# Kernel tuning notes

Hardware: AMD Instinct MI355X
Metric: run time of the kernel (lower is better)

## Reference

```python
import jax, jax.numpy as jnp
import numpy as np

EMBED = 256
HEADS = 8
LEVELS = 4
POINTS = 8
CAMS = 6
D_HEAD = EMBED // HEADS  # 32
SHAPES = [(92, 160), (46, 80), (23, 40), (12, 20)]  # (H, W) per level, L = 19560


def setup_inputs() -> dict:
    key = jax.random.key(0)
    ks = jax.random.split(key, 12)
    bs, nq, Z = 1, 2500, 4
    L = sum(h * w for h, w in SHAPES)

    def lin(k, fan_in, fan_out, scale=1.0):
        return jax.random.normal(k, (fan_in, fan_out), jnp.float32) * (scale / np.sqrt(fan_in).astype(np.float32))

    return dict(
        query=jax.random.normal(ks[0], (bs, nq, EMBED), jnp.float32),
        key_feats=jax.random.normal(ks[1], (CAMS, L, bs, EMBED), jnp.float32),
        reference_points_cam=jax.random.uniform(ks[2], (CAMS, bs, nq, Z, 2), jnp.float32),
        bev_mask=jax.random.bernoulli(ks[3], 0.3, (CAMS, bs, nq, Z)),
        spatial_shapes=jnp.array(SHAPES, dtype=jnp.int32),
        W_value=lin(ks[4], EMBED, EMBED),
        b_value=jnp.zeros((EMBED,), jnp.float32),
        W_off=lin(ks[5], EMBED, HEADS * LEVELS * POINTS * 2, 0.1),
        b_off=jnp.zeros((HEADS * LEVELS * POINTS * 2,), jnp.float32),
        W_attn=lin(ks[6], EMBED, HEADS * LEVELS * POINTS),
        b_attn=jnp.zeros((HEADS * LEVELS * POINTS,), jnp.float32),
        W_out=lin(ks[7], EMBED, EMBED),
        b_out=jnp.zeros((EMBED,), jnp.float32),
    )


def _deform_attn(q, val, ref, W_off, b_off, W_attn, b_attn):
    """MSDeformableAttention3D core. q: (Bc,Nq,C), val: (Bc,L,H,d) [already value-projected],
    ref: (Bc,Nq,Z,2) normalized camera-plane points."""
    Bc, Nq, C = q.shape
    Z = ref.shape[2]
    # sampling offsets, normalized per level by (W, H)
    off = (q @ W_off + b_off).reshape(Bc, Nq, HEADS, LEVELS, POINTS, 2)
    norm = jnp.array([[w, h] for h, w in SHAPES], jnp.float32)  # (Lv, 2) as (W, H)
    off = off / norm[None, None, None, :, None, :]
    # BEVFormer 3D combination: broadcast offsets over the Z pillar anchors
    off = off.reshape(Bc, Nq, HEADS, LEVELS, POINTS // Z, Z, 2)
    loc = ref[:, :, None, None, None, :, :] + off  # (Bc,Nq,H,Lv,P/Z,Z,2)
    loc = loc.reshape(Bc, Nq, HEADS, LEVELS, POINTS, 2)
    # attention weights softmaxed jointly over (levels*points)
    aw = jax.nn.softmax((q @ W_attn + b_attn).reshape(Bc, Nq, HEADS, LEVELS * POINTS), axis=-1)
    aw = aw.reshape(Bc, Nq, HEADS, LEVELS, POINTS)

    val_t = val.transpose(0, 2, 1, 3)  # (Bc,H,L,d)
    gather = jax.vmap(jax.vmap(lambda vm, im: vm[im]))  # over Bc and H
    out = jnp.zeros((Bc, HEADS, Nq, D_HEAD), jnp.float32)
    start = 0
    for lvl, (Hh, Ww) in enumerate(SHAPES):
        v_l = val_t[:, :, start:start + Hh * Ww]  # (Bc,H,HW,d)
        start += Hh * Ww
        # grid_sample semantics, align_corners=False, zero padding
        x = loc[:, :, :, lvl, :, 0] * Ww - 0.5  # (Bc,Nq,H,P)
        y = loc[:, :, :, lvl, :, 1] * Hh - 0.5
        x0 = jnp.floor(x)
        y0 = jnp.floor(y)
        fx = x - x0
        fy = y - y0
        a_l = aw[:, :, :, lvl]  # (Bc,Nq,H,P)
        for dy in (0, 1):
            for dx in (0, 1):
                xi = x0 + dx
                yi = y0 + dy
                wgt = (fx if dx else 1.0 - fx) * (fy if dy else 1.0 - fy)
                valid = (xi >= 0) & (xi < Ww) & (yi >= 0) & (yi < Hh)
                idx = (jnp.clip(yi, 0, Hh - 1) * Ww + jnp.clip(xi, 0, Ww - 1)).astype(jnp.int32)
                cw = jnp.where(valid, wgt * a_l, 0.0).transpose(0, 2, 1, 3)  # (Bc,H,Nq,P)
                g = gather(v_l, idx.transpose(0, 2, 1, 3))  # (Bc,H,Nq,P,d)
                out = out + jnp.einsum('bhnp,bhnpd->bhnd', cw, g)
    return out.transpose(0, 2, 1, 3).reshape(Bc, Nq, C)


def reference(query, key_feats, reference_points_cam, bev_mask, spatial_shapes,
              W_value, b_value, W_off, b_off, W_attn, b_attn, W_out, b_out):
    bs, nq, C = query.shape
    # Rebatch equivalent: every camera sees all queries; invalid ones are masked out
    # after the (fully per-query) deformable attention, which matches the original
    # gather->pad->attend->scatter math exactly.
    q_bc = jnp.broadcast_to(query[:, None], (bs, CAMS, nq, C)).reshape(bs * CAMS, nq, C)
    v = key_feats.transpose(2, 0, 1, 3).reshape(bs * CAMS, -1, C)  # (Bc,L,C)
    val = (v @ W_value + b_value).reshape(bs * CAMS, -1, HEADS, D_HEAD)
    ref = reference_points_cam.transpose(1, 0, 2, 3, 4).reshape(bs * CAMS, nq, -1, 2)
    out = _deform_attn(q_bc, val, ref, W_off, b_off, W_attn, b_attn)  # (Bc,nq,C)
    out = out.reshape(bs, CAMS, nq, C)
    valid_q = bev_mask.sum(-1) > 0  # (CAMS, bs, nq)
    mask = valid_q.transpose(1, 0, 2).astype(query.dtype)  # (bs, CAMS, nq)
    slots = jnp.einsum('bcq,bcqd->bqd', mask, out)
    count = jnp.maximum(mask.sum(1), 1.0)  # (bs, nq)
    slots = slots / count[..., None]
    return slots @ W_out + b_out + query
```

## Files before the change

### kernel.cpp

```cpp
#include <hip/hip_runtime.h>
#include <hip/hip_bf16.h>
#include <cstdint>

#define NCAMS 6
#define NQ 2500
#define EMBED 256
#define HEADS 8
#define DHEAD 32
#define LTOT 19560
#define MVAL (NCAMS * LTOT)

typedef __attribute__((ext_vector_type(8))) short bf16x8;
typedef __attribute__((ext_vector_type(4))) float f32x4;

__device__ __forceinline__ unsigned short f2bf(float f) {
  unsigned u = __float_as_uint(f);
  return (unsigned short)((u + 0x7fffu + ((u >> 16) & 1u)) >> 16);
}
__device__ __forceinline__ unsigned short bfbits(float x) {
  __hip_bfloat16 h = __float2bfloat16(x);
  return __builtin_bit_cast(unsigned short, h);
}
__device__ __forceinline__ void gl16(const unsigned short* g, unsigned short* l) {
  __builtin_amdgcn_global_load_lds(
      (const __attribute__((address_space(1))) unsigned int*)g,
      (__attribute__((address_space(3))) unsigned int*)l, 16, 0, 0);
}

__global__ __launch_bounds__(256) void k_prep(
    const float* __restrict__ Wv, const float* __restrict__ Woff,
    const float* __restrict__ Wattn, const float* __restrict__ Wout,
    const float* __restrict__ query,
    unsigned short* __restrict__ WT, unsigned short* __restrict__ WTq,
    unsigned short* __restrict__ WoutT, unsigned short* __restrict__ qbf)
{
  const int b = blockIdx.x, t = threadIdx.x;
  if (b < 256) {
    WT[(size_t)b * 256 + t] = f2bf(Wv[(size_t)t * 256 + b]);
  } else if (b < 768) {
    int c = b - 256;
    WTq[(size_t)c * 256 + t] = f2bf(Woff[(size_t)t * 512 + c]);
  } else if (b < 1024) {
    int c = b - 768;
    WTq[(size_t)(512 + c) * 256 + t] = f2bf(Wattn[(size_t)t * 256 + c]);
  } else if (b < 1280) {
    int c = b - 1024;
    WoutT[(size_t)c * 256 + t] = f2bf(Wout[(size_t)t * 256 + c]);
  } else {
    int q = b - 1280;
    qbf[(size_t)q * 256 + t] = f2bf(query[(size_t)q * 256 + t]);
  }
}

__global__ __launch_bounds__(256) void k_abf(
    const float* __restrict__ A, unsigned short* __restrict__ Abf)
{
  const size_t N8 = (size_t)MVAL * 256 / 8;
  for (size_t i = (size_t)blockIdx.x * 256 + threadIdx.x; i < N8;
       i += (size_t)gridDim.x * 256) {
    float4 x = *(const float4*)&A[i * 8];
    float4 y = *(const float4*)&A[i * 8 + 4];
    uint4 u;
    u.x = (unsigned)f2bf(x.x) | ((unsigned)f2bf(x.y) << 16);
    u.y = (unsigned)f2bf(x.z) | ((unsigned)f2bf(x.w) << 16);
    u.z = (unsigned)f2bf(y.x) | ((unsigned)f2bf(y.y) << 16);
    u.w = (unsigned)f2bf(y.z) | ((unsigned)f2bf(y.w) << 16);
    *(uint4*)&Abf[i * 8] = u;
  }
}

__global__ __launch_bounds__(512, 2) void k_valproj(
    const unsigned short* __restrict__ Abf,
    const unsigned short* __restrict__ WT,
    const float* __restrict__ bv,
    unsigned short* __restrict__ val)
{
  __shared__ unsigned short smem[128 * 64 + 256 * 64];
  unsigned short* As = smem;
  unsigned short* Bs = smem + 128 * 64;
  const int t = threadIdx.x;
  const int lane = t & 63;
  const int wid = t >> 6;
  const int wm = wid >> 2, wn = wid & 3;
  const int laneM = lane & 15, kGrp = lane >> 4;
  const int bm = blockIdx.x * 128;

  const int sub = t >> 3;
  const int swz = (t & 7) ^ (sub & 7);
  const unsigned short* aS0 = Abf + (size_t)min(bm + sub, MVAL - 1) * 256 + swz * 8;
  const unsigned short* aS1 = Abf + (size_t)min(bm + 64 + sub, MVAL - 1) * 256 + swz * 8;
  const unsigned short* bS0 = WT + (size_t)(sub) * 256 + swz * 8;
  const unsigned short* bS1 = WT + (size_t)(64 + sub) * 256 + swz * 8;
  const unsigned short* bS2 = WT + (size_t)(128 + sub) * 256 + swz * 8;
  const unsigned short* bS3 = WT + (size_t)(192 + sub) * 256 + swz * 8;

  f32x4 acc[4][4];
#pragma unroll
  for (int m = 0; m < 4; ++m)
#pragma unroll
    for (int n = 0; n < 4; ++n) acc[m][n] = {0.f, 0.f, 0.f, 0.f};

#pragma unroll 1
  for (int kk = 0; kk < 4; ++kk) {
    if (kk) __syncthreads();
    const int ko = kk * 64;
    gl16(aS0 + ko, As + wid * 512);
    gl16(aS1 + ko, As + 4096 + wid * 512);
    gl16(bS0 + ko, Bs + wid * 512);
    gl16(bS1 + ko, Bs + 4096 + wid * 512);
    gl16(bS2 + ko, Bs + 8192 + wid * 512);
    gl16(bS3 + ko, Bs + 12288 + wid * 512);
    __syncthreads();

#pragma unroll
    for (int ks = 0; ks < 2; ++ks) {
      bf16x8 af[4], bfr[4];
#pragma unroll
      for (int m = 0; m < 4; ++m) {
        int row = wm * 64 + m * 16 + laneM;
        af[m] = *(bf16x8*)&As[row * 64 + (((ks * 4 + kGrp) ^ (row & 7)) << 3)];
      }
#pragma unroll
      for (int n = 0; n < 4; ++n) {
        int row = wn * 64 + n * 16 + laneM;
        bfr[n] = *(bf16x8*)&Bs[row * 64 + (((ks * 4 + kGrp) ^ (row & 7)) << 3)];
      }
#pragma unroll
      for (int m = 0; m < 4; ++m)
#pragma unroll
        for (int n = 0; n < 4; ++n)
          acc[m][n] = __builtin_amdgcn_mfma_f32_16x16x32_bf16(bfr[n], af[m], acc[m][n], 0, 0, 0);
    }
  }

  float4 bb4[4];
#pragma unroll
  for (int n = 0; n < 4; ++n)
    bb4[n] = *(const float4*)&bv[wn * 64 + n * 16 + kGrp * 4];

  __syncthreads();
  unsigned short* tlw = smem + wid * (32 * 72);

#pragma unroll
  for (int hm = 0; hm < 2; ++hm) {
#pragma unroll
    for (int mm = 0; mm < 2; ++mm) {
      const int m = hm * 2 + mm;
#pragma unroll
      for (int n = 0; n < 4; ++n) {
        uint2 u;
        u.x = (unsigned)bfbits(acc[m][n][0] + bb4[n].x) |
              ((unsigned)bfbits(acc[m][n][1] + bb4[n].y) << 16);
        u.y = (unsigned)bfbits(acc[m][n][2] + bb4[n].z) |
              ((unsigned)bfbits(acc[m][n][3] + bb4[n].w) << 16);
        *(uint2*)&tlw[(mm * 16 + laneM) * 72 + n * 16 + kGrp * 4] = u;
      }
    }
#pragma unroll
    for (int i = 0; i < 4; ++i) {
      const int rowl = i * 8 + (lane >> 3);
      const int c8 = lane & 7;
      uint4 v = *(const uint4*)&tlw[rowl * 72 + c8 * 8];
      const int row = bm + wm * 64 + hm * 32 + rowl;
      if (row < MVAL)
        *(uint4*)&val[(size_t)row * 256 + wn * 64 + c8 * 8] = v;
    }
  }
}

__global__ __launch_bounds__(256, 2) void k_gemm_small(
    const unsigned short* __restrict__ A,
    const unsigned short* __restrict__ BT,
    const float* __restrict__ ba, const float* __restrict__ bb, int bsplit,
    const float* __restrict__ resid,
    float* __restrict__ C, int M, int N, int withResid)
{
  __shared__ unsigned short As[128 * 64];
  __shared__ unsigned short Bs[128 * 64];
  const int t = threadIdx.x;
  const int lane = t & 63;
  const int wid = t >> 6;
  const int wm = wid >> 1, wn = wid & 1;
  const int laneM = lane & 15, kGrp = lane >> 4;
  const int bm = blockIdx.x * 128;
  const int bn = blockIdx.y * 128;

  const int aC = t & 7, aR0 = t >> 3;

  uint4 aRegs[2][4];
  uint4 bRegs[2][4];
  f32x4 acc[4][4];
#pragma unroll
  for (int m = 0; m < 4; ++m)
#pragma unroll
    for (int n = 0; n < 4; ++n) acc[m][n] = {0.f, 0.f, 0.f, 0.f};

#pragma unroll
  for (int p = 0; p < 4; ++p) {
    int arow = bm + aR0 + p * 32;
    aRegs[0][p] = (arow < M) ? *(const uint4*)&A[(size_t)arow * 256 + aC * 8]
                             : make_uint4(0u, 0u, 0u, 0u);
    bRegs[0][p] = *(const uint4*)&BT[(size_t)(bn + aR0 + p * 32) * 256 + aC * 8];
  }

#pragma unroll
  for (int kk = 0; kk < 4; ++kk) {
    const int cur = kk & 1, nxt = cur ^ 1;
    if (kk) __syncthreads();
#pragma unroll
    for (int p = 0; p < 4; ++p) {
      int row = aR0 + p * 32;
      int elem = row * 64 + ((aC ^ (row & 7)) << 3);
      *(uint4*)&As[elem] = aRegs[cur][p];
      *(uint4*)&Bs[elem] = bRegs[cur][p];
    }
    __syncthreads();
    if (kk < 3) {
      const int kn = (kk + 1) * 64;
#pragma unroll
      for (int p = 0; p < 4; ++p) {
        int arow = bm + aR0 + p * 32;
        aRegs[nxt][p] = (arow < M)
            ? *(const uint4*)&A[(size_t)arow * 256 + kn + aC * 8]
            : make_uint4(0u, 0u, 0u, 0u);
        bRegs[nxt][p] = *(const uint4*)&BT[(size_t)(bn + aR0 + p * 32) * 256 + kn + aC * 8];
      }
    }
#pragma unroll
    for (int ks = 0; ks < 2; ++ks) {
      bf16x8 af[4], bfr[4];
#pragma unroll
      for (int m = 0; m < 4; ++m) {
        int row = wm * 64 + m * 16 + laneM;
        af[m] = *(bf16x8*)&As[row * 64 + (((ks * 4 + kGrp) ^ (row & 7)) << 3)];
      }
#pragma unroll
      for (int n = 0; n < 4; ++n) {
        int row = wn * 64 + n * 16 + laneM;
        bfr[n] = *(bf16x8*)&Bs[row * 64 + (((ks * 4 + kGrp) ^ (row & 7)) << 3)];
      }
#pragma unroll
      for (int m = 0; m < 4; ++m)
#pragma unroll
        for (int n = 0; n < 4; ++n)
          acc[m][n] = __builtin_amdgcn_mfma_f32_16x16x32_bf16(af[m], bfr[n], acc[m][n], 0, 0, 0);
    }
  }

  float bvn[4];
#pragma unroll
  for (int n = 0; n < 4; ++n) {
    int col = bn + wn * 64 + n * 16 + laneM;
    bvn[n] = (col < bsplit) ? ba[col] : bb[col - bsplit];
  }
#pragma unroll
  for (int m = 0; m < 4; ++m) {
#pragma unroll
    for (int r = 0; r < 4; ++r) {
      int row = bm + wm * 64 + m * 16 + kGrp * 4 + r;
      if (row < M) {
#pragma unroll
        for (int n = 0; n < 4; ++n) {
          int col = bn + wn * 64 + n * 16 + laneM;
          float v = acc[m][n][r] + bvn[n];
          if (withResid) v += resid[(size_t)row * 256 + col];
          C[(size_t)row * N + col] = v;
        }
      }
    }
  }
}

__global__ __launch_bounds__(256) void k_maskvalid(
    const unsigned char* __restrict__ MSK,
    unsigned char* __restrict__ valid)
{
  __shared__ int s_u8;
  const int t = threadIdx.x;
  if (t == 0) s_u8 = 0;
  __syncthreads();
  if ((t & 3) && MSK[t]) atomicOr(&s_u8, 1);
  __syncthreads();
  const int isU8 = s_u8;

  const int i = blockIdx.x * 256 + t;
  if (i < NCAMS * NQ) {
    int any;
    if (isU8) {
      const unsigned char* p = MSK + (size_t)i * 4;
      any = p[0] | p[1] | p[2] | p[3];
    } else {
      const int* p = (const int*)MSK + (size_t)i * 4;
      any = p[0] | p[1] | p[2] | p[3];
    }
    valid[i] = any ? 1 : 0;
  }
}

__global__ __launch_bounds__(256) void k_sample(
    const unsigned short* __restrict__ val,
    const float* __restrict__ OFFLOG,
    const float* __restrict__ REF,
    const unsigned char* __restrict__ valid,
    unsigned short* __restrict__ slots)
{
  __shared__ int2  s_pack[4][NCAMS][256];
  __shared__ float s_off[512];
  __shared__ float s_ref[48];
  __shared__ int   s_valid[6];

  const int q = blockIdx.x;
  const int t = threadIdx.x;

  s_off[t]       = OFFLOG[(size_t)q * 768 + t];
  s_off[t + 256] = OFFLOG[(size_t)q * 768 + 256 + t];
  if (t < 48) s_ref[t] = REF[(size_t)(t >> 3) * (NQ * 8) + (size_t)q * 8 + (t & 7)];
  if (t < 6) s_valid[t] = valid[(size_t)t * NQ + q];

  float logit = OFFLOG[(size_t)q * 768 + 512 + t];
  float m = logit;
#pragma unroll
  for (int o = 16; o > 0; o >>= 1) m = fmaxf(m, __shfl_xor(m, o, 32));
  float e = __expf(logit - m);
  float s = e;
#pragma unroll
  for (int o = 16; o > 0; o >>= 1) s += __shfl_xor(s, o, 32);
  const float a = e / s;
  __syncthreads();

  {
    const int h1 = t >> 5, lp = t & 31, lvl = lp >> 3, p = lp & 7, z = p & 3;
    const int WW = 160 >> lvl;
    const int HH = (lvl < 3) ? (92 >> lvl) : 12;
    const int S  = (lvl == 0) ? 0 : (lvl == 1) ? 14720 : (lvl == 2) ? 18400 : 19320;
    const float Wf = (float)WW, Hf = (float)HH;
    const float ox = s_off[h1 * 64 + lp * 2];
    const float oy = s_off[h1 * 64 + lp * 2 + 1];
#pragma unroll 1
    for (int cam = 0; cam < NCAMS; ++cam) {
      if (!s_valid[cam]) continue;
      float rx = s_ref[cam * 8 + z * 2];
      float ry = s_ref[cam * 8 + z * 2 + 1];
      float x = rx * Wf + ox - 0.5f;
      float y = ry * Hf + oy - 0.5f;
      float x0f = floorf(x), y0f = floorf(y);
      float fx = x - x0f, fy = y - y0f;
      int x0 = (int)x0f, y0 = (int)y0f;
      int base = cam * LTOT + S;
#pragma unroll
      for (int dy = 0; dy < 2; ++dy) {
        int yi = y0 + dy;
        float wy = dy ? fy : 1.f - fy;
        int yc = min(max(yi, 0), HH - 1);
        bool vy = (yi >= 0) && (yi < HH);
#pragma unroll
        for (int dx = 0; dx < 2; ++dx) {
          int xi = x0 + dx;
          float wx = dx ? fx : 1.f - fx;
          int xc = min(max(xi, 0), WW - 1);
          bool vv = vy && (xi >= 0) && (xi < WW);
          float wgt = vv ? wx * wy * a : 0.f;
          int addr = (base + yc * WW + xc) * 512;
          s_pack[dy * 2 + dx][cam][t] = make_int2(addr, __float_as_int(wgt));
        }
      }
    }
  }
  __syncthreads();

  const int h = t >> 5, pp = (t >> 3) & 3, l8 = t & 7;
  const unsigned dconst = (unsigned)(h * 64 + l8 * 8);
  const char* vb = (const char*)val;
  int nvalid = s_valid[0] + s_valid[1] + s_valid[2] + s_valid[3] + s_valid[4] + s_valid[5];
  float inv = 1.f / fmaxf((float)nvalid, 1.f);

  f32x4 acc = {0.f, 0.f, 0.f, 0.f};
#pragma unroll 1
  for (int cam = 0; cam < NCAMS; ++cam) {
    if (!s_valid[cam]) continue;
#pragma unroll
    for (int it = 0; it < 8; ++it) {
      const int idx = h * 32 + pp + it * 4;
      int2 pk0 = s_pack[0][cam][idx];
      int2 pk1 = s_pack[1][cam][idx];
      int2 pk2 = s_pack[2][cam][idx];
      int2 pk3 = s_pack[3][cam][idx];
      uint2 v0 = *(const uint2*)(vb + (size_t)((unsigned)pk0.x + dconst));
      uint2 v1 = *(const uint2*)(vb + (size_t)((unsigned)pk1.x + dconst));
      uint2 v2 = *(const uint2*)(vb + (size_t)((unsigned)pk2.x + dconst));
      uint2 v3 = *(const uint2*)(vb + (size_t)((unsigned)pk3.x + dconst));
      float w0 = __int_as_float(pk0.y), w1 = __int_as_float(pk1.y);
      float w2 = __int_as_float(pk2.y), w3 = __int_as_float(pk3.y);
      acc[0] += w0 * __uint_as_float(v0.x << 16);
      acc[1] += w0 * __uint_as_float(v0.x & 0xffff0000u);
      acc[2] += w0 * __uint_as_float(v0.y << 16);
      acc[3] += w0 * __uint_as_float(v0.y & 0xffff0000u);
      acc[0] += w1 * __uint_as_float(v1.x << 16);
      acc[1] += w1 * __uint_as_float(v1.x & 0xffff0000u);
      acc[2] += w1 * __uint_as_float(v1.y << 16);
      acc[3] += w1 * __uint_as_float(v1.y & 0xffff0000u);
      acc[0] += w2 * __uint_as_float(v2.x << 16);
      acc[1] += w2 * __uint_as_float(v2.x & 0xffff0000u);
      acc[2] += w2 * __uint_as_float(v2.y << 16);
      acc[3] += w2 * __uint_as_float(v2.y & 0xffff0000u);
      acc[0] += w3 * __uint_as_float(v3.x << 16);
      acc[1] += w3 * __uint_as_float(v3.x & 0xffff0000u);
      acc[2] += w3 * __uint_as_float(v3.y << 16);
      acc[3] += w3 * __uint_as_float(v3.y & 0xffff0000u);
    }
  }

#pragma unroll
  for (int i = 0; i < 4; ++i) {
    acc[i] += __shfl_xor(acc[i], 8);
    acc[i] += __shfl_xor(acc[i], 16);
  }
  if (pp == 0) {
    uint2 r;
    r.x = (unsigned)f2bf(acc[0] * inv) | ((unsigned)f2bf(acc[1] * inv) << 16);
    r.y = (unsigned)f2bf(acc[2] * inv) | ((unsigned)f2bf(acc[3] * inv) << 16);
    *(uint2*)&slots[(size_t)q * 256 + h * 32 + l8 * 4] = r;
  }
}

extern "C" void kernel_launch(void* const* d_in, const int* in_sizes, int n_in,
                              void* d_out, int out_size, void* d_ws, size_t ws_size,
                              hipStream_t stream) {
  const float* query     = (const float*)d_in[0];
  const float* key_feats = (const float*)d_in[1];
  const float* ref       = (const float*)d_in[2];
  const unsigned char* mask = (const unsigned char*)d_in[3];
  const float* Wv    = (const float*)d_in[5];
  const float* bv    = (const float*)d_in[6];
  const float* Woff  = (const float*)d_in[7];
  const float* boff  = (const float*)d_in[8];
  const float* Wattn = (const float*)d_in[9];
  const float* battn = (const float*)d_in[10];
  const float* Wout  = (const float*)d_in[11];
  const float* bout  = (const float*)d_in[12];
  float* out = (float*)d_out;

  char* ws = (char*)d_ws;
  size_t off = 0;
  unsigned short* val   = (unsigned short*)(ws + off); off += (size_t)MVAL * 256 * 2;
  unsigned short* WT    = (unsigned short*)(ws + off); off += 256 * 256 * 2;
  unsigned short* WTq   = (unsigned short*)(ws + off); off += 768 * 256 * 2;
  unsigned short* WoutT = (unsigned short*)(ws + off); off += 256 * 256 * 2;
  unsigned short* qbf   = (unsigned short*)(ws + off); off += (size_t)NQ * 256 * 2;
  float* OFFLOG = (float*)(ws + off); off += (size_t)NQ * 768 * 4;
  unsigned short* slots = (unsigned short*)(ws + off); off += (size_t)NQ * 256 * 2;
  unsigned char* valid  = (unsigned char*)(ws + off); off += NCAMS * NQ;

  hipLaunchKernelGGL(k_prep, dim3(1280 + NQ), dim3(256), 0, stream,
                     Wv, Woff, Wattn, Wout, query, WT, WTq, WoutT, qbf);
  hipLaunchKernelGGL(k_abf, dim3(2048), dim3(256), 0, stream,
                     key_feats, val);
  hipLaunchKernelGGL(k_valproj, dim3((MVAL + 127) / 128), dim3(512), 0, stream,
                     val, WT, bv, val);
  hipLaunchKernelGGL(k_gemm_small, dim3((NQ + 127) / 128, 6), dim3(256), 0, stream,
                     qbf, WTq, boff, battn, 512, (const float*)nullptr, OFFLOG, NQ, 768, 0);
  hipLaunchKernelGGL(k_maskvalid, dim3((NCAMS * NQ + 255) / 256), dim3(256), 0, stream,
                     mask, valid);
  hipLaunchKernelGGL(k_sample, dim3(NQ), dim3(256), 0, stream,
                     val, OFFLOG, ref, valid, slots);
  hipLaunchKernelGGL(k_gemm_small, dim3((NQ + 127) / 128, 2), dim3(256), 0, stream,
                     slots, WoutT, bout, bout, 1 << 30, query, out, NQ, 256, 1);
}
```

Baseline: 168.8 us.

## Fuse fp32-to-bf16 conversion into value projection GEMM and merge mask kernel into prep

The separate pass that converted key features to bf16 is removed. The value-projection GEMM now loads fp32 tiles straight into LDS with a swizzle and converts them to bf16 in registers before the MFMA. This avoids writing and re-reading an intermediate bf16 copy of the large key tensor. The mask-validity kernel is folded into the prep kernel as extra blocks, saving a launch. In exchange, the GEMM moves twice the bytes through LDS per tile, does extra conversion work in its inner loop, and now asks for 4 blocks per CU in its launch bounds.

```diff
diff --git a/kernel.cpp b/kernel.cpp
--- a/kernel.cpp
+++ b/kernel.cpp
@@ -21,7 +21,7 @@
   __hip_bfloat16 h = __float2bfloat16(x);
   return __builtin_bit_cast(unsigned short, h);
 }
-__device__ __forceinline__ void gl16(const unsigned short* g, unsigned short* l) {
+__device__ __forceinline__ void gl16(const void* g, void* l) {
   __builtin_amdgcn_global_load_lds(
       (const __attribute__((address_space(1))) unsigned int*)g,
       (__attribute__((address_space(3))) unsigned int*)l, 16, 0, 0);
@@ -30,9 +30,10 @@
 __global__ __launch_bounds__(256) void k_prep(
     const float* __restrict__ Wv, const float* __restrict__ Woff,
     const float* __restrict__ Wattn, const float* __restrict__ Wout,
-    const float* __restrict__ query,
+    const float* __restrict__ query, const unsigned char* __restrict__ MSK,
     unsigned short* __restrict__ WT, unsigned short* __restrict__ WTq,
-    unsigned short* __restrict__ WoutT, unsigned short* __restrict__ qbf)
+    unsigned short* __restrict__ WoutT, unsigned short* __restrict__ qbf,
+    unsigned char* __restrict__ valid)
 {
   const int b = blockIdx.x, t = threadIdx.x;
   if (b < 256) {
@@ -46,38 +47,40 @@
   } else if (b < 1280) {
     int c = b - 1024;
     WoutT[(size_t)c * 256 + t] = f2bf(Wout[(size_t)t * 256 + c]);
-  } else {
+  } else if (b < 1280 + NQ) {
     int q = b - 1280;
     qbf[(size_t)q * 256 + t] = f2bf(query[(size_t)q * 256 + t]);
-  }
-}
-
-__global__ __launch_bounds__(256) void k_abf(
-    const float* __restrict__ A, unsigned short* __restrict__ Abf)
-{
-  const size_t N8 = (size_t)MVAL * 256 / 8;
-  for (size_t i = (size_t)blockIdx.x * 256 + threadIdx.x; i < N8;
-       i += (size_t)gridDim.x * 256) {
-    float4 x = *(const float4*)&A[i * 8];
-    float4 y = *(const float4*)&A[i * 8 + 4];
-    uint4 u;
-    u.x = (unsigned)f2bf(x.x) | ((unsigned)f2bf(x.y) << 16);
-    u.y = (unsigned)f2bf(x.z) | ((unsigned)f2bf(x.w) << 16);
-    u.z = (unsigned)f2bf(y.x) | ((unsigned)f2bf(y.y) << 16);
-    u.w = (unsigned)f2bf(y.z) | ((unsigned)f2bf(y.w) << 16);
-    *(uint4*)&Abf[i * 8] = u;
-  }
-}
-
-__global__ __launch_bounds__(512, 2) void k_valproj(
-    const unsigned short* __restrict__ Abf,
+  } else {
+    __shared__ int s_u8;
+    if (t == 0) s_u8 = 0;
+    __syncthreads();
+    if ((t & 3) && MSK[t]) atomicOr(&s_u8, 1);
+    __syncthreads();
+    const int isU8 = s_u8;
+    const int i = (b - 1280 - NQ) * 256 + t;
+    if (i < NCAMS * NQ) {
+      int any;
+      if (isU8) {
+        const unsigned char* p = MSK + (size_t)i * 4;
+        any = p[0] | p[1] | p[2] | p[3];
+      } else {
+        const int* p = (const int*)MSK + (size_t)i * 4;
+        any = p[0] | p[1] | p[2] | p[3];
+      }
+      valid[i] = any ? 1 : 0;
+    }
+  }
+}
+
+__global__ __launch_bounds__(512, 4) void k_valproj(
+    const float* __restrict__ A,
     const unsigned short* __restrict__ WT,
     const float* __restrict__ bv,
     unsigned short* __restrict__ val)
 {
-  __shared__ unsigned short smem[128 * 64 + 256 * 64];
-  unsigned short* As = smem;
-  unsigned short* Bs = smem + 128 * 64;
+  __shared__ unsigned int smemu[16384];
+  float* Af = (float*)smemu;
+  unsigned short* Bs = (unsigned short*)(smemu + 8192);
   const int t = threadIdx.x;
   const int lane = t & 63;
   const int wid = t >> 6;
@@ -85,14 +88,21 @@
   const int laneM = lane & 15, kGrp = lane >> 4;
   const int bm = blockIdx.x * 128;
 
+  const float* aS[4];
+#pragma unroll
+  for (int p = 0; p < 4; ++p) {
+    int g16 = (wid * 4 + p) * 64 + lane;
+    int row = g16 >> 4;
+    int gl  = g16 & 15;
+    int g   = gl ^ ((row & 7) << 1);
+    aS[p] = A + (size_t)min(bm + row, MVAL - 1) * 256 + g * 4;
+  }
   const int sub = t >> 3;
   const int swz = (t & 7) ^ (sub & 7);
-  const unsigned short* aS0 = Abf + (size_t)min(bm + sub, MVAL - 1) * 256 + swz * 8;
-  const unsigned short* aS1 = Abf + (size_t)min(bm + 64 + sub, MVAL - 1) * 256 + swz * 8;
-  const unsigned short* bS0 = WT + (size_t)(sub) * 256 + swz * 8;
-  const unsigned short* bS1 = WT + (size_t)(64 + sub) * 256 + swz * 8;
-  const unsigned short* bS2 = WT + (size_t)(128 + sub) * 256 + swz * 8;
-  const unsigned short* bS3 = WT + (size_t)(192 + sub) * 256 + swz * 8;
+  const unsigned short* bS[4];
+#pragma unroll
+  for (int p = 0; p < 4; ++p)
+    bS[p] = WT + (size_t)(p * 64 + sub) * 256 + swz * 8;
 
   f32x4 acc[4][4];
 #pragma unroll
@@ -103,13 +113,13 @@
 #pragma unroll 1
   for (int kk = 0; kk < 4; ++kk) {
     if (kk) __syncthreads();
-    const int ko = kk * 64;
-    gl16(aS0 + ko, As + wid * 512);
-    gl16(aS1 + ko, As + 4096 + wid * 512);
-    gl16(bS0 + ko, Bs + wid * 512);
-    gl16(bS1 + ko, Bs + 4096 + wid * 512);
-    gl16(bS2 + ko, Bs + 8192 + wid * 512);
-    gl16(bS3 + ko, Bs + 12288 + wid * 512);
+    const int koF = kk * 64;
+#pragma unroll
+    for (int p = 0; p < 4; ++p)
+      gl16(aS[p] + koF, Af + (wid * 4 + p) * 256);
+#pragma unroll
+    for (int p = 0; p < 4; ++p)
+      gl16(bS[p] + koF, Bs + p * 4096 + wid * 512);
     __syncthreads();
 
 #pragma unroll
@@ -118,7 +128,16 @@
 #pragma unroll
       for (int m = 0; m < 4; ++m) {
         int row = wm * 64 + m * 16 + laneM;
-        af[m] = *(bf16x8*)&As[row * 64 + (((ks * 4 + kGrp) ^ (row & 7)) << 3)];
+        int u = (ks * 4 + kGrp) ^ (row & 7);
+        const float* p8 = &Af[row * 64 + u * 8];
+        float4 x = *(const float4*)p8;
+        float4 y = *(const float4*)(p8 + 4);
+        union { bf16x8 v; unsigned short u16[8]; } c;
+        c.u16[0] = bfbits(x.x); c.u16[1] = bfbits(x.y);
+        c.u16[2] = bfbits(x.z); c.u16[3] = bfbits(x.w);
+        c.u16[4] = bfbits(y.x); c.u16[5] = bfbits(y.y);
+        c.u16[6] = bfbits(y.z); c.u16[7] = bfbits(y.w);
+        af[m] = c.v;
       }
 #pragma unroll
       for (int n = 0; n < 4; ++n) {
@@ -139,7 +158,7 @@
     bb4[n] = *(const float4*)&bv[wn * 64 + n * 16 + kGrp * 4];
 
   __syncthreads();
-  unsigned short* tlw = smem + wid * (32 * 72);
+  unsigned short* tlw = (unsigned short*)smemu + wid * (32 * 72);
 
 #pragma unroll
   for (int hm = 0; hm < 2; ++hm) {
@@ -268,32 +287,6 @@
         }
       }
     }
-  }
-}
-
-__global__ __launch_bounds__(256) void k_maskvalid(
-    const unsigned char* __restrict__ MSK,
-    unsigned char* __restrict__ valid)
-{
-  __shared__ int s_u8;
-  const int t = threadIdx.x;
-  if (t == 0) s_u8 = 0;
-  __syncthreads();
-  if ((t & 3) && MSK[t]) atomicOr(&s_u8, 1);
-  __syncthreads();
-  const int isU8 = s_u8;
-
-  const int i = blockIdx.x * 256 + t;
-  if (i < NCAMS * NQ) {
-    int any;
-    if (isU8) {
-      const unsigned char* p = MSK + (size_t)i * 4;
-      any = p[0] | p[1] | p[2] | p[3];
-    } else {
-      const int* p = (const int*)MSK + (size_t)i * 4;
-      any = p[0] | p[1] | p[2] | p[3];
-    }
-    valid[i] = any ? 1 : 0;
   }
 }
 
@@ -451,16 +444,13 @@
   unsigned short* slots = (unsigned short*)(ws + off); off += (size_t)NQ * 256 * 2;
   unsigned char* valid  = (unsigned char*)(ws + off); off += NCAMS * NQ;
 
-  hipLaunchKernelGGL(k_prep, dim3(1280 + NQ), dim3(256), 0, stream,
-                     Wv, Woff, Wattn, Wout, query, WT, WTq, WoutT, qbf);
-  hipLaunchKernelGGL(k_abf, dim3(2048), dim3(256), 0, stream,
-                     key_feats, val);
+  const int MASKBLKS = (NCAMS * NQ + 255) / 256;
+  hipLaunchKernelGGL(k_prep, dim3(1280 + NQ + MASKBLKS), dim3(256), 0, stream,
+                     Wv, Woff, Wattn, Wout, query, mask, WT, WTq, WoutT, qbf, valid);
   hipLaunchKernelGGL(k_valproj, dim3((MVAL + 127) / 128), dim3(512), 0, stream,
-                     val, WT, bv, val);
+                     key_feats, WT, bv, val);
   hipLaunchKernelGGL(k_gemm_small, dim3((NQ + 127) / 128, 6), dim3(256), 0, stream,
                      qbf, WTq, boff, battn, 512, (const float*)nullptr, OFFLOG, NQ, 768, 0);
-  hipLaunchKernelGGL(k_maskvalid, dim3((NCAMS * NQ + 255) / 256), dim3(256), 0, stream,
-                     mask, valid);
   hipLaunchKernelGGL(k_sample, dim3(NQ), dim3(256), 0, stream,
                      val, OFFLOG, ref, valid, slots);
   hipLaunchKernelGGL(k_gemm_small, dim3((NQ + 127) / 128, 2), dim3(256), 0, stream,
```

Result: no change. 166.6 us (-1.3%).
